# Optimization experiments

Hardware: AMD Instinct MI355X
Metric: run time of the kernel (lower is better)

Reference implementation:

```python
import jax, jax.numpy as jnp
import numpy as np

PAD = float(-2**32 + 1)
NUM_HEADS = 16
LN_EPS = 1e-5


def _split_heads(x, h):
    # torch.cat(torch.chunk(x, h, dim=2), dim=0): head-major stacking
    B, T, D = x.shape
    d = D // h
    return x.reshape(B, T, h, d).transpose(2, 0, 1, 3).reshape(h * B, T, d)


def _merge_heads(x, h):
    # torch.cat(torch.chunk(x, h, dim=0), dim=2)
    hB, T, d = x.shape
    B = hB // h
    return x.reshape(h, B, T, d).transpose(1, 2, 0, 3).reshape(B, T, h * d)


def setup_inputs() -> dict:
    key = jax.random.key(0)
    ks = jax.random.split(key, 12)
    B, T, D = 2, 2048, 1024
    s = 1.0 / np.sqrt(D)
    return {
        "q": jax.random.normal(ks[0], (B, T, D), jnp.float32),
        "k": jax.random.normal(ks[1], (B, T, D), jnp.float32),
        "v": jax.random.normal(ks[2], (B, T, D), jnp.float32),
        "mask": jax.random.randint(ks[3], (B, T), 0, 2, jnp.int32),
        "causality": 0,
        "edge_fea": jnp.zeros((1,), jnp.float32),
        "wq": jax.random.normal(ks[4], (D, D), jnp.float32) * s,
        "bq": jax.random.normal(ks[5], (D,), jnp.float32) * 0.01,
        "wk": jax.random.normal(ks[6], (D, D), jnp.float32) * s,
        "bk": jax.random.normal(ks[7], (D,), jnp.float32) * 0.01,
        "wv": jax.random.normal(ks[8], (D, D), jnp.float32) * s,
        "bv": jax.random.normal(ks[9], (D,), jnp.float32) * 0.01,
        "gamma": jnp.ones((D,), jnp.float32),
        "beta": jnp.zeros((D,), jnp.float32),
    }


def reference(q, k, v, mask, causality, edge_fea, wq, bq, wk, bk, wv, bv, gamma, beta):
    h = NUM_HEADS
    B, T, D = q.shape
    depth = D // h

    qh = _split_heads(q @ wq.T + bq, h)   # (h*B, T, depth)
    kh = _split_heads(k @ wk.T + bk, h)
    vh = _split_heads(v @ wv.T + bv, h)

    scores = jnp.einsum('ntd,nsd->nts', qh, kh) / jnp.sqrt(jnp.asarray(depth, qh.dtype))
    # key mask: repeat_interleave over dim 0 (batch-major), 1 => masked
    km = jnp.repeat(mask.astype(scores.dtype), h, axis=0)[:, None, :]  # (h*B,1,T)
    scores = scores + km * PAD
    if causality:
        tril = jnp.tril(jnp.ones((T, T), scores.dtype))
        scores = jnp.where(tril[None] == 0, jnp.full_like(scores, PAD), scores)
    attn = jax.nn.softmax(scores, axis=-1)
    ctx = jnp.einsum('nts,nsd->ntd', attn, vh)

    out = _merge_heads(ctx, h) + q  # dropout is identity in eval mode
    # LayerNorm over last dim
    mu = jnp.mean(out, axis=-1, keepdims=True)
    var = jnp.var(out, axis=-1, keepdims=True)
    out = (out - mu) / jnp.sqrt(var + LN_EPS) * gamma + beta
    return out
```

## Files before the change

### kernel.cpp

```cpp
#include <hip/hip_runtime.h>
#include <hip/hip_bf16.h>
#include <stdint.h>

#define B_ 2
#define T_ 2048
#define D_ 1024
#define H_ 16
#define DEPTH 64

typedef unsigned short u16;
typedef unsigned int u32;
typedef short bf16x8 __attribute__((ext_vector_type(8)));
typedef float f32x4 __attribute__((ext_vector_type(4)));
typedef float f32x16 __attribute__((ext_vector_type(16)));

#define MFMA16(a, b, c) __builtin_amdgcn_mfma_f32_16x16x32_bf16(a, b, c, 0, 0, 0)
#define MFMA32(a, b, c) __builtin_amdgcn_mfma_f32_32x32x16_bf16(a, b, c, 0, 0, 0)

#if __has_builtin(__builtin_amdgcn_exp2f)
#define EXP2(x) __builtin_amdgcn_exp2f(x)
#else
#define EXP2(x) __expf((x) * 0.6931471805599453f)
#endif

#define GLOAD_LDS(g, l)                                                      \
    __builtin_amdgcn_global_load_lds(                                        \
        (__attribute__((address_space(1))) void*)(g),                        \
        (__attribute__((address_space(3))) void*)(l), 16, 0, 0)

__device__ __forceinline__ float bf2f(u32 u) {
    union { u32 i; float f; } x; x.i = u << 16; return x.f;
}
__device__ __forceinline__ u16 f2bf(float f) {
    union { float f; u32 i; } x; x.f = f;
    u32 r = x.i + 0x7fffu + ((x.i >> 16) & 1u);
    return (u16)(r >> 16);
}
__device__ __forceinline__ uint2 pk4(float4 f) {
    return make_uint2((u32)f2bf(f.x) | ((u32)f2bf(f.y) << 16),
                      (u32)f2bf(f.z) | ((u32)f2bf(f.w) << 16));
}
__device__ __forceinline__ u32 cvtpk(float lo, float hi) {
    u32 r;
    asm("v_cvt_pk_bf16_f32 %0, %1, %2" : "=v"(r) : "v"(lo), "v"(hi));
    return r;
}
__device__ __forceinline__ bf16x8 pk_frag(u32 a, u32 b, u32 c, u32 d) {
    union { u32 u[4]; bf16x8 v; } x;
    x.u[0] = a; x.u[1] = b; x.u[2] = c; x.u[3] = d;
    return x.v;
}
__device__ __forceinline__ f32x16 zero16() {
    f32x16 z;
    #pragma unroll
    for (int i = 0; i < 16; ++i) z[i] = 0.f;
    return z;
}

__global__ __launch_bounds__(256) void conv_kernel(
    const float* __restrict__ s0, const float* __restrict__ s1, const float* __restrict__ s2,
    const float* __restrict__ s3, const float* __restrict__ s4, const float* __restrict__ s5,
    u16* __restrict__ xbf, u16* __restrict__ wbf)
{
    const int z = blockIdx.y;
    const float* src = (z == 0) ? s0 : (z == 1) ? s1 : (z == 2) ? s2
                     : (z == 3) ? s3 : (z == 4) ? s4 : s5;
    u16* dst = (z < 3) ? (xbf + (size_t)z * 4194304) : (wbf + (size_t)(z - 3) * 1048576);
    const size_t nel = (z < 3) ? 4194304u : 1048576u;
    for (size_t i = ((size_t)blockIdx.x * 256 + threadIdx.x) * 8; i < nel;
         i += (size_t)gridDim.x * 2048) {
        float4 a = *(const float4*)(src + i);
        float4 b = *(const float4*)(src + i + 4);
        uint2 lo = pk4(a), hi = pk4(b);
        *(uint4*)(dst + i) = make_uint4(lo.x, lo.y, hi.x, hi.y);
    }
}

__global__ __launch_bounds__(256, 3) void proj_mfma(
    const u16* __restrict__ xbf, const u16* __restrict__ wbf,
    const float* __restrict__ bq, const float* __restrict__ bk, const float* __restrict__ bv,
    u16* __restrict__ qh, u16* __restrict__ kh, u16* __restrict__ vt)
{
    __shared__ __attribute__((aligned(16))) u16 SH[128 * 132];
    u16* As = SH;
    u16* Bs = SH + 8192;

    const int z = blockIdx.z;
    const u16* A = xbf + (size_t)z * 4194304;
    const u16* W = wbf + (size_t)z * 1048576;
    const float* bias = (z == 0) ? bq : (z == 1) ? bk : bv;

    const int tid = threadIdx.x, w = tid >> 6, lane = tid & 63;
    const int quad = lane >> 4, l16 = lane & 15;
    const int m0 = blockIdx.y * 128, n0 = blockIdx.x * 128;
    const int wm = (w & 1) * 64, wn = (w >> 1) * 64;
    const int srow = lane >> 3;
    const int schunk = (lane & 7) ^ srow;

    f32x4 acc[4][4];
    #pragma unroll
    for (int mi = 0; mi < 4; ++mi)
        #pragma unroll
        for (int ni = 0; ni < 4; ++ni) acc[mi][ni] = (f32x4){0.f, 0.f, 0.f, 0.f};

    const size_t ar = (size_t)(m0 + 32 * w + srow);
    const size_t br = (size_t)(n0 + 32 * w + srow);

    for (int k0 = 0; k0 < D_; k0 += 64) {
        __syncthreads();
        #pragma unroll
        for (int i = 0; i < 4; ++i) {
            GLOAD_LDS(A + (ar + 8 * i) * D_ + k0 + schunk * 8, &As[(32 * w + 8 * i) * 64]);
            GLOAD_LDS(W + (br + 8 * i) * D_ + k0 + schunk * 8, &Bs[(32 * w + 8 * i) * 64]);
        }
        __syncthreads();

        #pragma unroll
        for (int kg = 0; kg < 2; ++kg) {
            const int ch = ((4 * kg + quad) ^ (l16 & 7)) * 8;
            bf16x8 af[4], bf[4];
            #pragma unroll
            for (int mi = 0; mi < 4; ++mi)
                af[mi] = *(const bf16x8*)&As[(wm + 16 * mi + l16) * 64 + ch];
            #pragma unroll
            for (int ni = 0; ni < 4; ++ni)
                bf[ni] = *(const bf16x8*)&Bs[(wn + 16 * ni + l16) * 64 + ch];
            #pragma unroll
            for (int mi = 0; mi < 4; ++mi)
                #pragma unroll
                for (int ni = 0; ni < 4; ++ni)
                    acc[mi][ni] = MFMA16(af[mi], bf[ni], acc[mi][ni]);
        }
    }

    float bl[4];
    #pragma unroll
    for (int ni = 0; ni < 4; ++ni) bl[ni] = bias[n0 + wn + ni * 16 + l16];

    __syncthreads();

    if (z < 2) {
        #pragma unroll
        for (int mi = 0; mi < 4; ++mi) {
            #pragma unroll
            for (int ni = 0; ni < 4; ++ni) {
                const int nn = wn + ni * 16 + l16;
                #pragma unroll
                for (int r = 0; r < 4; ++r) {
                    const int tl = wm + mi * 16 + quad * 4 + r;
                    SH[tl * 132 + nn] = f2bf(acc[mi][ni][r] + bl[ni]);
                }
            }
        }
    } else {
        #pragma unroll
        for (int mi = 0; mi < 4; ++mi) {
            const int t4 = wm + mi * 16 + quad * 4;
            const int tp4 = (t4 & ~12) | ((t4 & 4) << 1) | ((t4 & 8) >> 1);
            #pragma unroll
            for (int ni = 0; ni < 4; ++ni) {
                const int nn = wn + ni * 16 + l16;
                float4 f = make_float4(acc[mi][ni][0] + bl[ni], acc[mi][ni][1] + bl[ni],
                                       acc[mi][ni][2] + bl[ni], acc[mi][ni][3] + bl[ni]);
                *(uint2*)&SH[nn * 132 + tp4] = pk4(f);
            }
        }
    }
    __syncthreads();

    {
        const int ch = tid & 31;
        const int r0 = tid >> 5;
        const int b  = m0 >> 11;
        const int tb = m0 & (T_ - 1);
        if (z < 2) {
            u16* outp = (z == 0) ? qh : kh;
            const int hd = ch >> 4;
            const int head = (n0 >> 6) + hd;
            const int dd = (ch & 15) * 4;
            #pragma unroll
            for (int s = 0; s < 16; ++s) {
                const int tl = r0 + s * 8;
                uint2 vv = *(const uint2*)&SH[tl * 132 + hd * 64 + dd];
                *(uint2*)(outp + ((size_t)(head * B_ + b) * T_ + tb + tl) * DEPTH + dd) = vv;
            }
        } else {
            #pragma unroll
            for (int s = 0; s < 16; ++s) {
                const int nn = r0 + s * 8;
                const int nng = n0 + nn;
                const int head = nng >> 6, d = nng & 63;
                uint2 vv = *(const uint2*)&SH[nn * 132 + ch * 4];
                *(uint2*)(vt + ((size_t)(head * B_ + b) * DEPTH + d) * T_ + tb + ch * 4) = vv;
            }
        }
    }
}

__global__ __launch_bounds__(256, 4) void attn_kernel(
    const u16* __restrict__ qh, const u16* __restrict__ kh, const u16* __restrict__ vt,
    const int* __restrict__ maskp, const int* __restrict__ causp,
    u16* __restrict__ po, float* __restrict__ pl)
{
    __shared__ __attribute__((aligned(16))) u16 Ks[2][64 * 64];
    __shared__ __attribute__((aligned(16))) u16 Vs[2][64 * 64];
    __shared__ __attribute__((aligned(16))) float padf[1024];

    const int lin = blockIdx.x + 16 * blockIdx.y + 512 * blockIdx.z;
    const int swz = (lin & 7) * 128 + (lin >> 3);
    const int qt = swz & 15;
    const int n  = (swz >> 4) & 31;
    const int kk = swz >> 9;

    const int kbase = kk * 1024;
    const int head = n >> 1, bi = n & 1;
    const int mrow = n >> 4;
    const int caus = causp[0];

    const int tid  = threadIdx.x;
    const int w    = tid >> 6, lane = tid & 63;
    const int l32  = lane & 31, h = lane >> 5;
    const size_t base  = (size_t)n * T_ * DEPTH;
    const size_t vbase = (size_t)n * DEPTH * T_;
    const size_t elems = (size_t)B_ * T_ * D_;

    const float C1  = 0.18033688011112042f;
    const float PL2 = -6.2e9f;

    {
        const int i0 = tid * 4;
        int4 m = *(const int4*)(maskp + (size_t)mrow * T_ + kbase + i0);
        padf[i0 + 0] = (float)m.x * PL2; padf[i0 + 1] = (float)m.y * PL2;
        padf[i0 + 2] = (float)m.z * PL2; padf[i0 + 3] = (float)m.w * PL2;
    }

    const int qg = qt * 128 + w * 32 + l32;
    bf16x8 aq[4];
    #pragma unroll
    for (int c = 0; c < 4; ++c)
        aq[c] = *(const bf16x8*)(qh + base + (size_t)qg * DEPTH + c * 16 + h * 8);

    f32x16 O0 = zero16(), O1 = zero16();
    float lp = 0.f;

    const int g_row = w * 16 + (lane >> 3);
    const int g_ch  = (lane & 7) ^ ((lane >> 3) & 7);
    const u16* ksrc = kh + base + (size_t)g_row * DEPTH + g_ch * 8;
    const u16* vsrc = vt + vbase + (size_t)g_row * T_ + g_ch * 8;

#define STAGE(bf_, t0_)                                                           \
    do {                                                                          \
        GLOAD_LDS(ksrc + (size_t)(t0_) * DEPTH,       &Ks[bf_][(w * 16) * 64]);   \
        GLOAD_LDS(ksrc + (size_t)((t0_) + 8) * DEPTH, &Ks[bf_][(w * 16 + 8) * 64]); \
        GLOAD_LDS(vsrc + (t0_),                       &Vs[bf_][(w * 16) * 64]);   \
        GLOAD_LDS(vsrc + (size_t)8 * T_ + (t0_),      &Vs[bf_][(w * 16 + 8) * 64]); \
    } while (0)

    STAGE(0, kbase);
    __syncthreads();

    for (int it = 0; it < 16; ++it) {
        const int cur = it & 1;
        if (it < 15) STAGE(cur ^ 1, kbase + (it + 1) * 64);

        const int lt0 = it * 64;
        bf16x8 pa[2][2];
        #pragma unroll
        for (int kb = 0; kb < 2; ++kb) {
            const int krow = kb * 32 + l32;
            const u16* krp = &Ks[cur][krow * 64];
            const int ksw = krow & 7;
            f32x16 st = zero16();
            #pragma unroll
            for (int c = 0; c < 4; ++c) {
                bf16x8 kf = *(const bf16x8*)(krp + (((c * 2 + h) ^ ksw) * 8));
                st = MFMA32(kf, aq[c], st);
            }
            u32 pk[8];
            #pragma unroll
            for (int g = 0; g < 4; ++g) {
                f32x4 pv = *(const f32x4*)&padf[lt0 + kb * 32 + g * 8 + h * 4];
                #pragma unroll
                for (int m2 = 0; m2 < 2; ++m2) {
                    const int r0 = g * 4 + m2 * 2;
                    float v0 = fmaf(st[r0],     C1, pv[m2 * 2]);
                    float v1 = fmaf(st[r0 + 1], C1, pv[m2 * 2 + 1]);
                    if (caus) {
                        const int kg = kbase + lt0 + kb * 32 + g * 8 + h * 4 + m2 * 2;
                        if (kg     > qg) v0 = PL2;
                        if (kg + 1 > qg) v1 = PL2;
                    }
                    const float e0 = EXP2(v0), e1 = EXP2(v1);
                    lp += e0 + e1;
                    pk[g * 2 + m2] = cvtpk(e0, e1);
                }
            }
            pa[kb][0] = pk_frag(pk[0], pk[1], pk[2], pk[3]);
            pa[kb][1] = pk_frag(pk[4], pk[5], pk[6], pk[7]);
        }

        #pragma unroll
        for (int dblk = 0; dblk < 2; ++dblk) {
            const int d = dblk * 32 + l32;
            const u16* vrp = &Vs[cur][d * 64];
            const int vsw = d & 7;
            #pragma unroll
            for (int kb = 0; kb < 2; ++kb)
                #pragma unroll
                for (int kc = 0; kc < 2; ++kc) {
                    const int ch = (kb * 4 + kc * 2 + h) ^ vsw;
                    bf16x8 vf = *(const bf16x8*)(vrp + ch * 8);
                    if (dblk == 0) O0 = MFMA32(pa[kb][kc], vf, O0);
                    else           O1 = MFMA32(pa[kb][kc], vf, O1);
                }
        }

        __syncthreads();
    }
#undef STAGE

    lp += __shfl_xor(lp, 32, 64);
    u16* pop = po + (size_t)kk * elems;
    float* plp = pl + (size_t)kk * 32 * T_;
    if (lane < 32)
        plp[(size_t)n * T_ + qt * 128 + w * 32 + l32] = lp;

    #pragma unroll
    for (int r = 0; r < 16; ++r) {
        const int q = qt * 128 + w * 32 + (r & 3) + 8 * (r >> 2) + 4 * h;
        const size_t rb = ((size_t)bi * T_ + q) * D_ + head * DEPTH + l32;
        pop[rb]      = f2bf(O0[r]);
        pop[rb + 32] = f2bf(O1[r]);
    }
}

__global__ __launch_bounds__(256) void fuse_ln(
    const u16* __restrict__ po, const float* __restrict__ pl,
    const float* __restrict__ qin,
    const float* __restrict__ gamma, const float* __restrict__ beta,
    float* __restrict__ out)
{
    const int row = blockIdx.x;
    const int bi = row >> 11, t = row & (T_ - 1);
    const int tid = threadIdx.x;
    const size_t elems = (size_t)B_ * T_ * D_;

    const int head = tid >> 4;
    const size_t li = (size_t)(head * B_ + bi) * T_ + t;
    const float l = pl[li] + pl[32 * T_ + li];
    const float inv = 1.0f / fmaxf(l, 1e-30f);

    const size_t basei = (size_t)row * D_ + (tid << 2);
    uint2 a = *(const uint2*)(po + basei);
    uint2 b = *(const uint2*)(po + elems + basei);
    float4 qv = *(const float4*)(qin + basei);
    float x[4];
    x[0] = (bf2f(a.x & 0xffffu) + bf2f(b.x & 0xffffu)) * inv + qv.x;
    x[1] = (bf2f(a.x >> 16)     + bf2f(b.x >> 16))     * inv + qv.y;
    x[2] = (bf2f(a.y & 0xffffu) + bf2f(b.y & 0xffffu)) * inv + qv.z;
    x[3] = (bf2f(a.y >> 16)     + bf2f(b.y >> 16))     * inv + qv.w;

    float s  = x[0] + x[1] + x[2] + x[3];
    float s2 = x[0]*x[0] + x[1]*x[1] + x[2]*x[2] + x[3]*x[3];
    #pragma unroll
    for (int off = 1; off < 64; off <<= 1) {
        s  += __shfl_xor(s, off, 64);
        s2 += __shfl_xor(s2, off, 64);
    }
    __shared__ float rs[4], rs2[4];
    const int wid = tid >> 6;
    if ((tid & 63) == 0) { rs[wid] = s; rs2[wid] = s2; }
    __syncthreads();
    s  = rs[0] + rs[1] + rs[2] + rs[3];
    s2 = rs2[0] + rs2[1] + rs2[2] + rs2[3];
    const float mean = s * (1.0f / (float)D_);
    const float var  = s2 * (1.0f / (float)D_) - mean * mean;
    const float rstd = rsqrtf(var + 1e-5f);
    float4 g = *(const float4*)(gamma + (tid << 2));
    float4 bb = *(const float4*)(beta + (tid << 2));
    float4 r;
    r.x = (x[0] - mean) * rstd * g.x + bb.x;
    r.y = (x[1] - mean) * rstd * g.y + bb.y;
    r.z = (x[2] - mean) * rstd * g.z + bb.z;
    r.w = (x[3] - mean) * rstd * g.w + bb.w;
    *(float4*)(out + basei) = r;
}

extern "C" void kernel_launch(void* const* d_in, const int* in_sizes, int n_in,
                              void* d_out, int out_size, void* d_ws, size_t ws_size,
                              hipStream_t stream)
{
    (void)in_sizes; (void)n_in; (void)out_size; (void)ws_size;
    const float* q    = (const float*)d_in[0];
    const float* k    = (const float*)d_in[1];
    const float* v    = (const float*)d_in[2];
    const int* mask = (const int*)d_in[3];
    const int* caus = (const int*)d_in[4];
    const float* wq = (const float*)d_in[6];
    const float* bq = (const float*)d_in[7];
    const float* wk = (const float*)d_in[8];
    const float* bk = (const float*)d_in[9];
    const float* wv = (const float*)d_in[10];
    const float* bv = (const float*)d_in[11];
    const float* gamma = (const float*)d_in[12];
    const float* beta  = (const float*)d_in[13];
    float* out = (float*)d_out;

    const size_t elems = (size_t)B_ * T_ * D_;
    u16* qh  = (u16*)d_ws;
    u16* kh  = qh + elems;
    u16* vt  = kh + elems;
    u16* xbf = vt + elems;
    u16* wbf = xbf + 3 * elems;
    u16* po   = xbf;
    float* pl = (float*)(po + 2 * elems);

    conv_kernel<<<dim3(512, 6), 256, 0, stream>>>(q, k, v, wq, wk, wv, xbf, wbf);
    proj_mfma<<<dim3(8, 32, 3), 256, 0, stream>>>(xbf, wbf, bq, bk, bv, qh, kh, vt);

    dim3 agrid(T_ / 128, H_ * B_, 2);
    attn_kernel<<<agrid, 256, 0, stream>>>(qh, kh, vt, mask, caus, po, pl);

    fuse_ln<<<B_ * T_, 256, 0, stream>>>(po, pl, q, gamma, beta, out);
}
```

Before: 211.6 us.

## Fuse fp32-to-bf16 activation conversion into projection GEMM tile loads

The separate conversion pass over q/k/v activations is removed. The projection kernel now reads fp32 activations directly, converts them to bf16 in registers and stores them to swizzled LDS, while only the weights are still pre-converted. This avoids writing and re-reading a 24MB bf16 activation buffer. In exchange, each activation tile is fetched as fp32 by all 8 column blocks, which doubles the A-side bytes in the GEMM, and the loads go synchronously through registers instead of direct global-to-LDS loads.

```diff
diff --git a/kernel.cpp b/kernel.cpp
--- a/kernel.cpp
+++ b/kernel.cpp
@@ -57,17 +57,14 @@
     return z;
 }
 
-__global__ __launch_bounds__(256) void conv_kernel(
+__global__ __launch_bounds__(256) void convw_kernel(
     const float* __restrict__ s0, const float* __restrict__ s1, const float* __restrict__ s2,
-    const float* __restrict__ s3, const float* __restrict__ s4, const float* __restrict__ s5,
-    u16* __restrict__ xbf, u16* __restrict__ wbf)
+    u16* __restrict__ wbf)
 {
     const int z = blockIdx.y;
-    const float* src = (z == 0) ? s0 : (z == 1) ? s1 : (z == 2) ? s2
-                     : (z == 3) ? s3 : (z == 4) ? s4 : s5;
-    u16* dst = (z < 3) ? (xbf + (size_t)z * 4194304) : (wbf + (size_t)(z - 3) * 1048576);
-    const size_t nel = (z < 3) ? 4194304u : 1048576u;
-    for (size_t i = ((size_t)blockIdx.x * 256 + threadIdx.x) * 8; i < nel;
+    const float* src = (z == 0) ? s0 : (z == 1) ? s1 : s2;
+    u16* dst = wbf + (size_t)z * 1048576;
+    for (size_t i = ((size_t)blockIdx.x * 256 + threadIdx.x) * 8; i < 1048576u;
          i += (size_t)gridDim.x * 2048) {
         float4 a = *(const float4*)(src + i);
         float4 b = *(const float4*)(src + i + 4);
@@ -77,7 +74,8 @@
 }
 
 __global__ __launch_bounds__(256, 3) void proj_mfma(
-    const u16* __restrict__ xbf, const u16* __restrict__ wbf,
+    const float* __restrict__ qf, const float* __restrict__ kf, const float* __restrict__ vf,
+    const u16* __restrict__ wbf,
     const float* __restrict__ bq, const float* __restrict__ bk, const float* __restrict__ bv,
     u16* __restrict__ qh, u16* __restrict__ kh, u16* __restrict__ vt)
 {
@@ -86,7 +84,7 @@
     u16* Bs = SH + 8192;
 
     const int z = blockIdx.z;
-    const u16* A = xbf + (size_t)z * 4194304;
+    const float* X = (z == 0) ? qf : (z == 1) ? kf : vf;
     const u16* W = wbf + (size_t)z * 1048576;
     const float* bias = (z == 0) ? bq : (z == 1) ? bk : bv;
 
@@ -97,21 +95,33 @@
     const int srow = lane >> 3;
     const int schunk = (lane & 7) ^ srow;
 
+    const int xr = tid >> 3;
+    const int xc = tid & 7;
+    const int xsw = (xc ^ (xr & 7)) * 8;
+
     f32x4 acc[4][4];
     #pragma unroll
     for (int mi = 0; mi < 4; ++mi)
         #pragma unroll
         for (int ni = 0; ni < 4; ++ni) acc[mi][ni] = (f32x4){0.f, 0.f, 0.f, 0.f};
 
-    const size_t ar = (size_t)(m0 + 32 * w + srow);
     const size_t br = (size_t)(n0 + 32 * w + srow);
 
     for (int k0 = 0; k0 < D_; k0 += 64) {
         __syncthreads();
         #pragma unroll
-        for (int i = 0; i < 4; ++i) {
-            GLOAD_LDS(A + (ar + 8 * i) * D_ + k0 + schunk * 8, &As[(32 * w + 8 * i) * 64]);
+        for (int i = 0; i < 4; ++i)
             GLOAD_LDS(W + (br + 8 * i) * D_ + k0 + schunk * 8, &Bs[(32 * w + 8 * i) * 64]);
+        #pragma unroll
+        for (int u = 0; u < 4; ++u) {
+            const int row = u * 32 + xr;
+            const float* p = X + (size_t)(m0 + row) * D_ + k0 + xc * 8;
+            float4 a0 = *(const float4*)p;
+            float4 a1 = *(const float4*)(p + 4);
+            uint4 pv;
+            pv.x = cvtpk(a0.x, a0.y); pv.y = cvtpk(a0.z, a0.w);
+            pv.z = cvtpk(a1.x, a1.y); pv.w = cvtpk(a1.z, a1.w);
+            *(uint4*)&As[row * 64 + xsw] = pv;
         }
         __syncthreads();
 
@@ -410,13 +420,12 @@
     u16* qh  = (u16*)d_ws;
     u16* kh  = qh + elems;
     u16* vt  = kh + elems;
-    u16* xbf = vt + elems;
-    u16* wbf = xbf + 3 * elems;
-    u16* po   = xbf;
+    u16* wbf = vt + elems;
+    u16* po  = wbf + 3 * 1048576;
     float* pl = (float*)(po + 2 * elems);
 
-    conv_kernel<<<dim3(512, 6), 256, 0, stream>>>(q, k, v, wq, wk, wv, xbf, wbf);
-    proj_mfma<<<dim3(8, 32, 3), 256, 0, stream>>>(xbf, wbf, bq, bk, bv, qh, kh, vt);
+    convw_kernel<<<dim3(64, 3), 256, 0, stream>>>(wq, wk, wv, wbf);
+    proj_mfma<<<dim3(8, 32, 3), 256, 0, stream>>>(q, k, v, wbf, bq, bk, bv, qh, kh, vt);
 
     dim3 agrid(T_ / 128, H_ * B_, 2);
     attn_kernel<<<agrid, 256, 0, stream>>>(qh, kh, vt, mask, caus, po, pl);
```

New measurement: 228.6 us. 8.0% more time.
